# Optimization experiments

Measured on AMD Instinct MI355X. Metric: run time of the kernel, lower is better.

Reference implementation:

```python
import jax, jax.numpy as jnp
import numpy as np

N_BLOCKS = 8
N_WIRES = 24
GAMMA, BETA, ALPHA = 0.1, 0.6, 0.15


def _apply_ry(state, w, theta):
    # RY(theta) = [[cos(t/2), -sin(t/2)], [sin(t/2), cos(t/2)]] on wire w.
    c = jnp.cos(theta * 0.5)
    s = jnp.sin(theta * 0.5)
    st = jnp.moveaxis(state, w, 0)  # (2, ...)
    new = jnp.stack([c * st[0] - s * st[1], s * st[0] + c * st[1]])
    return jnp.moveaxis(new, 0, w)


def _apply_cnot(state, ctrl, tgt):
    # Flip target bit where control bit == 1.
    st = jnp.moveaxis(state, (ctrl, tgt), (0, 1))  # (2, 2, ...)
    new = jnp.stack([st[0], st[1, ::-1]])
    return jnp.moveaxis(new, (0, 1), (ctrl, tgt))


def setup_inputs() -> dict:
    key = jax.random.key(0)
    angles = jax.random.normal(key, (N_BLOCKS, N_WIRES), dtype=jnp.float32)
    return {"angles": angles}


def reference(angles):
    n_blocks, n_wires = angles.shape  # static
    # Initial state |0...0>; RY and CNOT are real, so the state stays real.
    state = jnp.zeros((2,) * n_wires, dtype=angles.dtype).at[(0,) * n_wires].set(1.0)
    for k in range(n_blocks):
        for w in range(n_wires):
            state = _apply_ry(state, w, angles[k, w])
        for w in range(n_wires - 1):  # circular=False -> linear chain
            state = _apply_cnot(state, w, w + 1)
    probs = (state.reshape(-1) ** 2).reshape(2 ** n_wires, 1)  # |amp|^2
    easy_scale = 2.0 ** (n_wires - 1)
    x = (BETA * jnp.tanh(GAMMA * easy_scale * probs)) ** ALPHA
    return x - jnp.mean(x)
```

## Files before the change

kernel.cpp:

```cpp
#include <hip/hip_runtime.h>

#define NB 8
#define SSIZE (1u << 24)


__global__ void k_prep(const float* __restrict__ ang, float* __restrict__ ws) {
    int t = threadIdx.x;
    if (t == 0) ws[0] = 0.0f;
    if (t < NB * 24) {
        float a = 0.5f * ang[t];
        ws[64 + t]  = __builtin_cosf(a);
        ws[256 + t] = __builtin_sinf(a);
    }
}


__device__ __forceinline__ unsigned sw(unsigned f) {
    return f ^ (((f >> 3) ^ (f >> 5)) & 7u);
}

__device__ __forceinline__ void ry2(float& a0, float& a1, float c, float s, bool ctl) {
    float w0 = c * a0 - s * a1;
    float w1 = s * a0 + c * a1;
    a0 = ctl ? w1 : w0;
    a1 = ctl ? w0 : w1;
}

template<int TB, int MODE>
__device__ __forceinline__ void stage8(float4* x, float c, float s) {
#pragma unroll
    for (int j0 = 0; j0 < 8; ++j0) {
        if (j0 & (1 << TB)) continue;
        const int j1 = j0 | (1 << TB);
        const bool ctl = (MODE == 1) || (MODE == 0 && ((j0 >> (TB + 1)) & 1));
        ry2(x[j0].x, x[j1].x, c, s, ctl);
        ry2(x[j0].y, x[j1].y, c, s, ctl);
        ry2(x[j0].z, x[j1].z, c, s, ctl);
        ry2(x[j0].w, x[j1].w, c, s, ctl);
    }
}

__device__ __forceinline__ void coefs(unsigned lane, int lb, bool g,
                                      float c, float s, float& cA, float& cP) {
    bool b = (lane >> lb) & 1u;
    cA = g ? (b ? -s : s) : c;
    cP = g ? c : (b ? s : -s);
}

__device__ __forceinline__ void lane_stage(float4* x, int mask, float cA, float cP) {
#pragma unroll
    for (int j = 0; j < 8; ++j) {
        float px = __shfl_xor(x[j].x, mask, 64);
        float py = __shfl_xor(x[j].y, mask, 64);
        float pz = __shfl_xor(x[j].z, mask, 64);
        float pw = __shfl_xor(x[j].w, mask, 64);
        x[j].x = cA * x[j].x + cP * px;
        x[j].y = cA * x[j].y + cP * py;
        x[j].z = cA * x[j].z + cP * pz;
        x[j].w = cA * x[j].w + cP * pw;
    }
}

__device__ __forceinline__ void lane_stage_jc(float4* x, int mask,
                                              float cA0, float cP0,
                                              float cA1, float cP1) {
#pragma unroll
    for (int j = 0; j < 8; ++j) {
        float cA = (j & 1) ? cA1 : cA0;
        float cP = (j & 1) ? cP1 : cP0;
        float px = __shfl_xor(x[j].x, mask, 64);
        float py = __shfl_xor(x[j].y, mask, 64);
        float pz = __shfl_xor(x[j].z, mask, 64);
        float pw = __shfl_xor(x[j].w, mask, 64);
        x[j].x = cA * x[j].x + cP * px;
        x[j].y = cA * x[j].y + cP * py;
        x[j].z = cA * x[j].z + cP * pz;
        x[j].w = cA * x[j].w + cP * pw;
    }
}

__device__ __forceinline__ void dstages(float4* x, float c1, float s1, bool g1,
                                        float c0, float s0) {
#pragma unroll
    for (int j = 0; j < 8; ++j) {
        ry2(x[j].x, x[j].z, c1, s1, g1);
        ry2(x[j].y, x[j].w, c1, s1, g1);
        ry2(x[j].x, x[j].y, c0, s0, false);
        ry2(x[j].z, x[j].w, c0, s0, true);
    }
}

__device__ __forceinline__ float xform(float v) {
    float z = 838860.8f * v * v;
    float e2 = __builtin_amdgcn_exp2f(z * 2.8853900817779268f);
    float big = 1.0f - 2.0f * __builtin_amdgcn_rcpf(e2 + 1.0f);
    float z2 = z * z;
    float small_ = z * (1.0f - 0.33333333f * z2 * (1.0f - 0.4f * z2));
    float t = (z < 0.04f) ? small_ : big;
    return __builtin_amdgcn_exp2f(0.15f * __builtin_amdgcn_logf(0.6f * t));
}

__global__ __launch_bounds__(512, 4) void k_passA(float* __restrict__ st,
                                                  float* __restrict__ ws,
                                                  int k, int fuse) {
    __shared__ float4 T4[4096];
    const unsigned m = blockIdx.x;
    const unsigned tid = threadIdx.x;
    const unsigned lane = tid & 63u;
    const float* C = ws + 64 + k * 24;
    const float* S = ws + 256 + k * 24;
    float ca[14], sa[14];
#pragma unroll
    for (int b = 0; b < 14; ++b) { ca[b] = C[23 - b]; sa[b] = S[23 - b]; }

    float4* G4 = reinterpret_cast<float4*>(st) + (m << 12);
    float4 x[8];

#pragma unroll
    for (int jj = 0; jj < 8; ++jj) x[jj] = G4[tid + (jj << 9)];
    if (m & 1u) stage8<2, 1>(x, ca[13], sa[13]);
    else        stage8<2,-1>(x, ca[13], sa[13]);
    stage8<1, 0>(x, ca[12], sa[12]);
    stage8<0, 0>(x, ca[11], sa[11]);
#pragma unroll
    for (int jj = 0; jj < 8; ++jj) T4[sw(tid | (jj << 9))] = x[jj];
    __syncthreads();
    const unsigned hi = (tid >> 6) << 9;
#pragma unroll
    for (int jj = 0; jj < 8; ++jj) x[jj] = T4[sw(lane | (jj << 6) | hi)];
    if (tid & 64u) stage8<2, 1>(x, ca[10], sa[10]);
    else           stage8<2,-1>(x, ca[10], sa[10]);
    stage8<1, 0>(x, ca[9], sa[9]);
    stage8<0, 0>(x, ca[8], sa[8]);
    {
        float cA0, cP0, cA1, cP1;
        coefs(lane, 5, false, ca[7], sa[7], cA0, cP0);
        coefs(lane, 5, true,  ca[7], sa[7], cA1, cP1);
        lane_stage_jc(x, 32, cA0, cP0, cA1, cP1);
    }
    { float cA, cP; coefs(lane, 4, (lane >> 5) & 1, ca[6], sa[6], cA, cP); lane_stage(x, 16, cA, cP); }
    { float cA, cP; coefs(lane, 3, (lane >> 4) & 1, ca[5], sa[5], cA, cP); lane_stage(x,  8, cA, cP); }
    { float cA, cP; coefs(lane, 2, (lane >> 3) & 1, ca[4], sa[4], cA, cP); lane_stage(x,  4, cA, cP); }
    { float cA, cP; coefs(lane, 1, (lane >> 2) & 1, ca[3], sa[3], cA, cP); lane_stage(x,  2, cA, cP); }
    { float cA, cP; coefs(lane, 0, (lane >> 1) & 1, ca[2], sa[2], cA, cP); lane_stage(x,  1, cA, cP); }
    dstages(x, ca[1], sa[1], lane & 1u, ca[0], sa[0]);

    if (fuse) {
        float lsum = 0.f;
#pragma unroll
        for (int jj = 0; jj < 8; ++jj) {
            float* v = &x[jj].x;
#pragma unroll
            for (int d = 0; d < 4; ++d) { v[d] = xform(v[d]); lsum += v[d]; }
        }
#pragma unroll
        for (int jj = 0; jj < 8; ++jj) G4[lane | (jj << 6) | hi] = x[jj];
#pragma unroll
        for (int o = 32; o > 0; o >>= 1) lsum += __shfl_down(lsum, o, 64);
        __syncthreads();
        float* wsum = reinterpret_cast<float*>(T4);
        if ((tid & 63u) == 0) wsum[tid >> 6] = lsum;
        __syncthreads();
        if (tid == 0) {
            float b = 0.f;
#pragma unroll
            for (int i = 0; i < 8; ++i) b += wsum[i];
            atomicAdd(ws, b);
        }
    } else {
#pragma unroll
        for (int jj = 0; jj < 8; ++jj) G4[lane | (jj << 6) | hi] = x[jj];
    }
}

__global__ __launch_bounds__(512, 4) void k_passB(float* __restrict__ st,
                                                  const float* __restrict__ ws,
                                                  int k, int init) {
    __shared__ float4 T4[4096];
    const unsigned m = blockIdx.x;
    const unsigned tid = threadIdx.x;
    const unsigned lane = tid & 63u;
    const float* C = ws + 64 + k * 24;
    const float* S = ws + 256 + k * 24;
    float cg[10], sg[10];
#pragma unroll
    for (int t = 0; t < 10; ++t) { cg[t] = C[9 - t]; sg[t] = S[9 - t]; }

    float4* G4 = reinterpret_cast<float4*>(st);
    const unsigned mb = m << 2;
    float4 x[8];

    if (init) {
        const float* C0 = ws + 64;
        const float* S0 = ws + 256;
        float P = 1.f;
        { unsigned g = (tid ^ (tid >> 1)) & 1u;        P *= g ? S0[21] : C0[21]; }
        { unsigned g = ((tid >> 1) ^ m) & 1u;          P *= g ? S0[20] : C0[20]; }
#pragma unroll
        for (int b = 4; b <= 12; ++b) {
            unsigned g = ((m >> (b - 4)) ^ (m >> (b - 3))) & 1u;
            P *= g ? S0[23 - b] : C0[23 - b];
        }
        { unsigned g = ((m >> 9) ^ (tid >> 2)) & 1u;   P *= g ? S0[10] : C0[10]; }
#pragma unroll
        for (int b = 14; b <= 19; ++b) {
            unsigned g = ((tid >> (b - 12)) ^ (tid >> (b - 11))) & 1u;
            P *= g ? S0[23 - b] : C0[23 - b];
        }
        float D[4];
#pragma unroll
        for (int d = 0; d < 4; ++d) {
            unsigned g0 = (d ^ (d >> 1)) & 1u;
            unsigned g1 = ((d >> 1) ^ tid) & 1u;
            D[d] = (g0 ? S0[23] : C0[23]) * (g1 ? S0[22] : C0[22]);
        }
        unsigned t8 = (tid >> 8) & 1u;
#pragma unroll
        for (int jj = 0; jj < 8; ++jj) {
            unsigned g20 = (t8 ^ (unsigned)jj) & 1u;
            unsigned g21 = ((unsigned)jj ^ ((unsigned)jj >> 1)) & 1u;
            unsigned g22 = (((unsigned)jj >> 1) ^ ((unsigned)jj >> 2)) & 1u;
            unsigned g23 = (((unsigned)jj >> 2)) & 1u;
            float J = (g20 ? S0[3] : C0[3]) * (g21 ? S0[2] : C0[2]) *
                      (g22 ? S0[1] : C0[1]) * (g23 ? S0[0] : C0[0]);
            float PJ = P * J;
            x[jj] = make_float4(PJ * D[0], PJ * D[1], PJ * D[2], PJ * D[3]);
        }
    } else {
#pragma unroll
        for (int jj = 0; jj < 8; ++jj) {
            unsigned lf = tid | (jj << 9);
            x[jj] = G4[(lf & 3u) | mb | ((lf >> 2) << 12)];
        }
    }
    stage8<2,-1>(x, cg[9], sg[9]);
    stage8<1, 0>(x, cg[8], sg[8]);
    stage8<0, 0>(x, cg[7], sg[7]);
#pragma unroll
    for (int jj = 0; jj < 8; ++jj) T4[sw(tid | (jj << 9))] = x[jj];
    __syncthreads();
    const unsigned hi = (tid >> 6) << 9;
#pragma unroll
    for (int jj = 0; jj < 8; ++jj) x[jj] = T4[sw(lane | (jj << 6) | hi)];
    if (tid & 64u) stage8<2, 1>(x, cg[6], sg[6]);
    else           stage8<2,-1>(x, cg[6], sg[6]);
    stage8<1, 0>(x, cg[5], sg[5]);
    stage8<0, 0>(x, cg[4], sg[4]);
    {
        float cA0, cP0, cA1, cP1;
        coefs(lane, 5, false, cg[3], sg[3], cA0, cP0);
        coefs(lane, 5, true,  cg[3], sg[3], cA1, cP1);
        lane_stage_jc(x, 32, cA0, cP0, cA1, cP1);
    }
    { float cA, cP; coefs(lane, 4, (lane >> 5) & 1, cg[2], sg[2], cA, cP); lane_stage(x, 16, cA, cP); }
    { float cA, cP; coefs(lane, 3, (lane >> 4) & 1, cg[1], sg[1], cA, cP); lane_stage(x,  8, cA, cP); }
    { float cA, cP; coefs(lane, 2, (lane >> 3) & 1, cg[0], sg[0], cA, cP); lane_stage(x,  4, cA, cP); }
#pragma unroll
    for (int jj = 0; jj < 8; ++jj) {
        unsigned lf = lane | (jj << 6) | hi;
        G4[(lf & 3u) | mb | ((lf >> 2) << 12)] = x[jj];
    }
}

__global__ void k_final(float* __restrict__ st, const float* __restrict__ ws) {
    unsigned idx = blockIdx.x * blockDim.x + threadIdx.x;
    unsigned stride = gridDim.x * blockDim.x;
    float mean = ws[0] * (1.0f / 16777216.0f);
    float4* G4 = reinterpret_cast<float4*>(st);
    for (unsigned q = idx; q < (SSIZE / 4); q += stride) {
        float4 v = G4[q];
        v.x -= mean; v.y -= mean; v.z -= mean; v.w -= mean;
        G4[q] = v;
    }
}

extern "C" void kernel_launch(void* const* d_in, const int* in_sizes, int n_in,
                              void* d_out, int out_size, void* d_ws, size_t ws_size,
                              hipStream_t stream) {
    const float* ang = (const float*)d_in[0];
    float* st = (float*)d_out;
    float* ws = (float*)d_ws;

    k_prep<<<1, 256, 0, stream>>>(ang, ws);
    for (int k = 1; k < NB; ++k) {
        k_passB<<<1024, 512, 0, stream>>>(st, ws, k, (k == 1) ? 1 : 0);
        k_passA<<<1024, 512, 0, stream>>>(st, ws, k, (k == NB - 1) ? 1 : 0);
    }
    k_final<<<4096, 256, 0, stream>>>(st, ws);
}
```

Baseline: 529.8 us.

## Fuse multiple circuit blocks per pass using light-cone ordering, with double-precision state

```diff
diff --git a/kernel.cpp b/kernel.cpp
--- a/kernel.cpp
+++ b/kernel.cpp
@@ -4,13 +4,13 @@
 #define SSIZE (1u << 24)
 
 
-__global__ void k_prep(const float* __restrict__ ang, float* __restrict__ ws) {
+__global__ void k_prep(const float* __restrict__ ang, double* __restrict__ dws) {
     int t = threadIdx.x;
-    if (t == 0) ws[0] = 0.0f;
+    if (t == 0) dws[0] = 0.0;
     if (t < NB * 24) {
-        float a = 0.5f * ang[t];
-        ws[64 + t]  = __builtin_cosf(a);
-        ws[256 + t] = __builtin_sinf(a);
+        double a = 0.5 * (double)ang[t];
+        dws[8 + t]   = cos(a);
+        dws[200 + t] = sin(a);
     }
 }
 
@@ -19,41 +19,41 @@
     return f ^ (((f >> 3) ^ (f >> 5)) & 7u);
 }
 
-__device__ __forceinline__ void ry2(float& a0, float& a1, float c, float s, bool ctl) {
-    float w0 = c * a0 - s * a1;
-    float w1 = s * a0 + c * a1;
+__device__ __forceinline__ void ry2d(double& a0, double& a1, double c, double s, bool ctl) {
+    double w0 = c * a0 - s * a1;
+    double w1 = s * a0 + c * a1;
     a0 = ctl ? w1 : w0;
     a1 = ctl ? w0 : w1;
 }
 
 template<int TB, int MODE>
-__device__ __forceinline__ void stage8(float4* x, float c, float s) {
+__device__ __forceinline__ void stage8d(double4* x, double c, double s) {
 #pragma unroll
     for (int j0 = 0; j0 < 8; ++j0) {
         if (j0 & (1 << TB)) continue;
         const int j1 = j0 | (1 << TB);
         const bool ctl = (MODE == 1) || (MODE == 0 && ((j0 >> (TB + 1)) & 1));
-        ry2(x[j0].x, x[j1].x, c, s, ctl);
-        ry2(x[j0].y, x[j1].y, c, s, ctl);
-        ry2(x[j0].z, x[j1].z, c, s, ctl);
-        ry2(x[j0].w, x[j1].w, c, s, ctl);
-    }
-}
-
-__device__ __forceinline__ void coefs(unsigned lane, int lb, bool g,
-                                      float c, float s, float& cA, float& cP) {
+        ry2d(x[j0].x, x[j1].x, c, s, ctl);
+        ry2d(x[j0].y, x[j1].y, c, s, ctl);
+        ry2d(x[j0].z, x[j1].z, c, s, ctl);
+        ry2d(x[j0].w, x[j1].w, c, s, ctl);
+    }
+}
+
+__device__ __forceinline__ void coefs_d(unsigned lane, int lb, bool g,
+                                        double c, double s, double& cA, double& cP) {
     bool b = (lane >> lb) & 1u;
     cA = g ? (b ? -s : s) : c;
     cP = g ? c : (b ? s : -s);
 }
 
-__device__ __forceinline__ void lane_stage(float4* x, int mask, float cA, float cP) {
+__device__ __forceinline__ void lane_stage_d(double4* x, int mask, double cA, double cP) {
 #pragma unroll
     for (int j = 0; j < 8; ++j) {
-        float px = __shfl_xor(x[j].x, mask, 64);
-        float py = __shfl_xor(x[j].y, mask, 64);
-        float pz = __shfl_xor(x[j].z, mask, 64);
-        float pw = __shfl_xor(x[j].w, mask, 64);
+        double px = __shfl_xor(x[j].x, mask, 64);
+        double py = __shfl_xor(x[j].y, mask, 64);
+        double pz = __shfl_xor(x[j].z, mask, 64);
+        double pw = __shfl_xor(x[j].w, mask, 64);
         x[j].x = cA * x[j].x + cP * px;
         x[j].y = cA * x[j].y + cP * py;
         x[j].z = cA * x[j].z + cP * pz;
@@ -61,17 +61,17 @@
     }
 }
 
-__device__ __forceinline__ void lane_stage_jc(float4* x, int mask,
-                                              float cA0, float cP0,
-                                              float cA1, float cP1) {
+__device__ __forceinline__ void lane_stage_jc_d(double4* x, int mask,
+                                                double cA0, double cP0,
+                                                double cA1, double cP1) {
 #pragma unroll
     for (int j = 0; j < 8; ++j) {
-        float cA = (j & 1) ? cA1 : cA0;
-        float cP = (j & 1) ? cP1 : cP0;
-        float px = __shfl_xor(x[j].x, mask, 64);
-        float py = __shfl_xor(x[j].y, mask, 64);
-        float pz = __shfl_xor(x[j].z, mask, 64);
-        float pw = __shfl_xor(x[j].w, mask, 64);
+        double cA = (j & 1) ? cA1 : cA0;
+        double cP = (j & 1) ? cP1 : cP0;
+        double px = __shfl_xor(x[j].x, mask, 64);
+        double py = __shfl_xor(x[j].y, mask, 64);
+        double pz = __shfl_xor(x[j].z, mask, 64);
+        double pw = __shfl_xor(x[j].w, mask, 64);
         x[j].x = cA * x[j].x + cP * px;
         x[j].y = cA * x[j].y + cP * py;
         x[j].z = cA * x[j].z + cP * pz;
@@ -79,19 +79,18 @@
     }
 }
 
-__device__ __forceinline__ void dstages(float4* x, float c1, float s1, bool g1,
-                                        float c0, float s0) {
+__device__ __forceinline__ void dstages_d(double4* x, double c1, double s1, bool g1,
+                                          double c0, double s0) {
 #pragma unroll
     for (int j = 0; j < 8; ++j) {
-        ry2(x[j].x, x[j].z, c1, s1, g1);
-        ry2(x[j].y, x[j].w, c1, s1, g1);
-        ry2(x[j].x, x[j].y, c0, s0, false);
-        ry2(x[j].z, x[j].w, c0, s0, true);
-    }
-}
-
-__device__ __forceinline__ float xform(float v) {
-    float z = 838860.8f * v * v;
+        ry2d(x[j].x, x[j].z, c1, s1, g1);
+        ry2d(x[j].y, x[j].w, c1, s1, g1);
+        ry2d(x[j].x, x[j].y, c0, s0, false);
+        ry2d(x[j].z, x[j].w, c0, s0, true);
+    }
+}
+
+__device__ __forceinline__ float xform(float z) {
     float e2 = __builtin_amdgcn_exp2f(z * 2.8853900817779268f);
     float big = 1.0f - 2.0f * __builtin_amdgcn_rcpf(e2 + 1.0f);
     float z2 = z * z;
@@ -100,118 +99,126 @@
     return __builtin_amdgcn_exp2f(0.15f * __builtin_amdgcn_logf(0.6f * t));
 }
 
-__global__ __launch_bounds__(512, 4) void k_passA(float* __restrict__ st,
-                                                  float* __restrict__ ws,
-                                                  int k, int fuse) {
+
+__device__ __forceinline__ float4 lo4(const double4 v) {
+    return make_float4(__int_as_float(__double2loint(v.x)),
+                       __int_as_float(__double2loint(v.y)),
+                       __int_as_float(__double2loint(v.z)),
+                       __int_as_float(__double2loint(v.w)));
+}
+__device__ __forceinline__ float4 hi4(const double4 v) {
+    return make_float4(__int_as_float(__double2hiint(v.x)),
+                       __int_as_float(__double2hiint(v.y)),
+                       __int_as_float(__double2hiint(v.z)),
+                       __int_as_float(__double2hiint(v.w)));
+}
+__device__ __forceinline__ double4 mk4(const float4 h, const float4 l) {
+    return make_double4(__hiloint2double(__float_as_int(h.x), __float_as_int(l.x)),
+                        __hiloint2double(__float_as_int(h.y), __float_as_int(l.y)),
+                        __hiloint2double(__float_as_int(h.z), __float_as_int(l.z)),
+                        __hiloint2double(__float_as_int(h.w), __float_as_int(l.w)));
+}
+
+__device__ __forceinline__ void t_fwd_d(float4* T4, double4* x, unsigned tid,
+                                        unsigned lane, unsigned hi, bool protect) {
+    if (protect) __syncthreads();
+#pragma unroll
+    for (int jj = 0; jj < 8; ++jj) T4[sw(tid | (jj << 9))] = lo4(x[jj]);
+    __syncthreads();
+    float4 tl[8];
+#pragma unroll
+    for (int jj = 0; jj < 8; ++jj) tl[jj] = T4[sw(lane | (jj << 6) | hi)];
+    __syncthreads();
+#pragma unroll
+    for (int jj = 0; jj < 8; ++jj) T4[sw(tid | (jj << 9))] = hi4(x[jj]);
+    __syncthreads();
+#pragma unroll
+    for (int jj = 0; jj < 8; ++jj)
+        x[jj] = mk4(T4[sw(lane | (jj << 6) | hi)], tl[jj]);
+}
+
+__device__ __forceinline__ void t_back_d(float4* T4, double4* x, unsigned tid,
+                                         unsigned lane, unsigned hi) {
+    __syncthreads();
+#pragma unroll
+    for (int jj = 0; jj < 8; ++jj) T4[sw(lane | (jj << 6) | hi)] = lo4(x[jj]);
+    __syncthreads();
+    float4 tl[8];
+#pragma unroll
+    for (int jj = 0; jj < 8; ++jj) tl[jj] = T4[sw(tid | (jj << 9))];
+    __syncthreads();
+#pragma unroll
+    for (int jj = 0; jj < 8; ++jj) T4[sw(lane | (jj << 6) | hi)] = hi4(x[jj]);
+    __syncthreads();
+#pragma unroll
+    for (int jj = 0; jj < 8; ++jj)
+        x[jj] = mk4(T4[sw(tid | (jj << 9))], tl[jj]);
+}
+
+__device__ __forceinline__ void jj_trio_d(double4* x, const double* c, const double* s,
+                                          bool top_on, int start) {
+    if (start == 0) {
+        if (top_on) stage8d<2, 1>(x, c[0], s[0]);
+        else        stage8d<2,-1>(x, c[0], s[0]);
+    }
+    if (start <= 1) stage8d<1, 0>(x, c[1], s[1]);
+    stage8d<0, 0>(x, c[2], s[2]);
+}
+
+__device__ __forceinline__ void lane_ladder_d(double4* x, unsigned lane,
+                                              const double* c, const double* s, int n) {
+    {
+        double cA0, cP0, cA1, cP1;
+        coefs_d(lane, 5, false, c[0], s[0], cA0, cP0);
+        coefs_d(lane, 5, true,  c[0], s[0], cA1, cP1);
+        lane_stage_jc_d(x, 32, cA0, cP0, cA1, cP1);
+    }
+    if (n > 1) { double cA, cP; coefs_d(lane, 4, (lane >> 5) & 1, c[1], s[1], cA, cP); lane_stage_d(x, 16, cA, cP); }
+    if (n > 2) { double cA, cP; coefs_d(lane, 3, (lane >> 4) & 1, c[2], s[2], cA, cP); lane_stage_d(x,  8, cA, cP); }
+    if (n > 3) { double cA, cP; coefs_d(lane, 2, (lane >> 3) & 1, c[3], s[3], cA, cP); lane_stage_d(x,  4, cA, cP); }
+    if (n > 4) { double cA, cP; coefs_d(lane, 1, (lane >> 2) & 1, c[4], s[4], cA, cP); lane_stage_d(x,  2, cA, cP); }
+    if (n > 5) { double cA, cP; coefs_d(lane, 0, (lane >> 1) & 1, c[5], s[5], cA, cP); lane_stage_d(x,  1, cA, cP); }
+}
+
+__device__ __forceinline__ double4 d4_of(const float4 f) {
+    return make_double4((double)f.x, (double)f.y, (double)f.z, (double)f.w);
+}
+__device__ __forceinline__ float4 f4_of(const double4 d) {
+    return make_float4((float)d.x, (float)d.y, (float)d.z, (float)d.w);
+}
+
+__global__ __launch_bounds__(512, 2) void k_H(float* __restrict__ st,
+                                              const double* __restrict__ dws,
+                                              int kbase, int nblk, int init) {
     __shared__ float4 T4[4096];
-    const unsigned m = blockIdx.x;
+    const unsigned bid = blockIdx.x;
+    const unsigned m = (bid >> 3) | ((bid & 7u) << 7);
     const unsigned tid = threadIdx.x;
     const unsigned lane = tid & 63u;
-    const float* C = ws + 64 + k * 24;
-    const float* S = ws + 256 + k * 24;
-    float ca[14], sa[14];
-#pragma unroll
-    for (int b = 0; b < 14; ++b) { ca[b] = C[23 - b]; sa[b] = S[23 - b]; }
-
-    float4* G4 = reinterpret_cast<float4*>(st) + (m << 12);
-    float4 x[8];
-
-#pragma unroll
-    for (int jj = 0; jj < 8; ++jj) x[jj] = G4[tid + (jj << 9)];
-    if (m & 1u) stage8<2, 1>(x, ca[13], sa[13]);
-    else        stage8<2,-1>(x, ca[13], sa[13]);
-    stage8<1, 0>(x, ca[12], sa[12]);
-    stage8<0, 0>(x, ca[11], sa[11]);
-#pragma unroll
-    for (int jj = 0; jj < 8; ++jj) T4[sw(tid | (jj << 9))] = x[jj];
-    __syncthreads();
     const unsigned hi = (tid >> 6) << 9;
-#pragma unroll
-    for (int jj = 0; jj < 8; ++jj) x[jj] = T4[sw(lane | (jj << 6) | hi)];
-    if (tid & 64u) stage8<2, 1>(x, ca[10], sa[10]);
-    else           stage8<2,-1>(x, ca[10], sa[10]);
-    stage8<1, 0>(x, ca[9], sa[9]);
-    stage8<0, 0>(x, ca[8], sa[8]);
-    {
-        float cA0, cP0, cA1, cP1;
-        coefs(lane, 5, false, ca[7], sa[7], cA0, cP0);
-        coefs(lane, 5, true,  ca[7], sa[7], cA1, cP1);
-        lane_stage_jc(x, 32, cA0, cP0, cA1, cP1);
-    }
-    { float cA, cP; coefs(lane, 4, (lane >> 5) & 1, ca[6], sa[6], cA, cP); lane_stage(x, 16, cA, cP); }
-    { float cA, cP; coefs(lane, 3, (lane >> 4) & 1, ca[5], sa[5], cA, cP); lane_stage(x,  8, cA, cP); }
-    { float cA, cP; coefs(lane, 2, (lane >> 3) & 1, ca[4], sa[4], cA, cP); lane_stage(x,  4, cA, cP); }
-    { float cA, cP; coefs(lane, 1, (lane >> 2) & 1, ca[3], sa[3], cA, cP); lane_stage(x,  2, cA, cP); }
-    { float cA, cP; coefs(lane, 0, (lane >> 1) & 1, ca[2], sa[2], cA, cP); lane_stage(x,  1, cA, cP); }
-    dstages(x, ca[1], sa[1], lane & 1u, ca[0], sa[0]);
-
-    if (fuse) {
-        float lsum = 0.f;
-#pragma unroll
-        for (int jj = 0; jj < 8; ++jj) {
-            float* v = &x[jj].x;
-#pragma unroll
-            for (int d = 0; d < 4; ++d) { v[d] = xform(v[d]); lsum += v[d]; }
-        }
-#pragma unroll
-        for (int jj = 0; jj < 8; ++jj) G4[lane | (jj << 6) | hi] = x[jj];
-#pragma unroll
-        for (int o = 32; o > 0; o >>= 1) lsum += __shfl_down(lsum, o, 64);
-        __syncthreads();
-        float* wsum = reinterpret_cast<float*>(T4);
-        if ((tid & 63u) == 0) wsum[tid >> 6] = lsum;
-        __syncthreads();
-        if (tid == 0) {
-            float b = 0.f;
-#pragma unroll
-            for (int i = 0; i < 8; ++i) b += wsum[i];
-            atomicAdd(ws, b);
-        }
-    } else {
-#pragma unroll
-        for (int jj = 0; jj < 8; ++jj) G4[lane | (jj << 6) | hi] = x[jj];
-    }
-}
-
-__global__ __launch_bounds__(512, 4) void k_passB(float* __restrict__ st,
-                                                  const float* __restrict__ ws,
-                                                  int k, int init) {
-    __shared__ float4 T4[4096];
-    const unsigned m = blockIdx.x;
-    const unsigned tid = threadIdx.x;
-    const unsigned lane = tid & 63u;
-    const float* C = ws + 64 + k * 24;
-    const float* S = ws + 256 + k * 24;
-    float cg[10], sg[10];
-#pragma unroll
-    for (int t = 0; t < 10; ++t) { cg[t] = C[9 - t]; sg[t] = S[9 - t]; }
-
     float4* G4 = reinterpret_cast<float4*>(st);
-    const unsigned mb = m << 2;
-    float4 x[8];
+    double4 x[8];
 
     if (init) {
-        const float* C0 = ws + 64;
-        const float* S0 = ws + 256;
-        float P = 1.f;
-        { unsigned g = (tid ^ (tid >> 1)) & 1u;        P *= g ? S0[21] : C0[21]; }
-        { unsigned g = ((tid >> 1) ^ m) & 1u;          P *= g ? S0[20] : C0[20]; }
-#pragma unroll
-        for (int b = 4; b <= 12; ++b) {
-            unsigned g = ((m >> (b - 4)) ^ (m >> (b - 3))) & 1u;
+        const double* C0 = dws + 8;
+        const double* S0 = dws + 200;
+        double P = 1.0;
+#pragma unroll
+        for (int b = 2; b <= 10; ++b) {
+            unsigned g = ((m >> (b - 2)) ^ (m >> (b - 1))) & 1u;
             P *= g ? S0[23 - b] : C0[23 - b];
         }
-        { unsigned g = ((m >> 9) ^ (tid >> 2)) & 1u;   P *= g ? S0[10] : C0[10]; }
-#pragma unroll
-        for (int b = 14; b <= 19; ++b) {
+        { unsigned g = ((m >> 9) ^ tid) & 1u; P *= g ? S0[12] : C0[12]; }
+#pragma unroll
+        for (int b = 12; b <= 19; ++b) {
             unsigned g = ((tid >> (b - 12)) ^ (tid >> (b - 11))) & 1u;
             P *= g ? S0[23 - b] : C0[23 - b];
         }
-        float D[4];
+        double D[4];
 #pragma unroll
         for (int d = 0; d < 4; ++d) {
             unsigned g0 = (d ^ (d >> 1)) & 1u;
-            unsigned g1 = ((d >> 1) ^ tid) & 1u;
+            unsigned g1 = ((d >> 1) ^ m) & 1u;
             D[d] = (g0 ? S0[23] : C0[23]) * (g1 ? S0[22] : C0[22]);
         }
         unsigned t8 = (tid >> 8) & 1u;
@@ -221,51 +228,97 @@
             unsigned g21 = ((unsigned)jj ^ ((unsigned)jj >> 1)) & 1u;
             unsigned g22 = (((unsigned)jj >> 1) ^ ((unsigned)jj >> 2)) & 1u;
             unsigned g23 = (((unsigned)jj >> 2)) & 1u;
-            float J = (g20 ? S0[3] : C0[3]) * (g21 ? S0[2] : C0[2]) *
-                      (g22 ? S0[1] : C0[1]) * (g23 ? S0[0] : C0[0]);
-            float PJ = P * J;
-            x[jj] = make_float4(PJ * D[0], PJ * D[1], PJ * D[2], PJ * D[3]);
+            double J = (g20 ? S0[3] : C0[3]) * (g21 ? S0[2] : C0[2]) *
+                       (g22 ? S0[1] : C0[1]) * (g23 ? S0[0] : C0[0]);
+            double PJ = P * J;
+            x[jj] = make_double4(PJ * D[0], PJ * D[1], PJ * D[2], PJ * D[3]);
         }
     } else {
 #pragma unroll
         for (int jj = 0; jj < 8; ++jj) {
-            unsigned lf = tid | (jj << 9);
-            x[jj] = G4[(lf & 3u) | mb | ((lf >> 2) << 12)];
-        }
-    }
-    stage8<2,-1>(x, cg[9], sg[9]);
-    stage8<1, 0>(x, cg[8], sg[8]);
-    stage8<0, 0>(x, cg[7], sg[7]);
-#pragma unroll
-    for (int jj = 0; jj < 8; ++jj) T4[sw(tid | (jj << 9))] = x[jj];
-    __syncthreads();
+            unsigned w = tid | (jj << 9);
+            x[jj] = d4_of(G4[m | (w << 10)]);
+        }
+    }
+
+    for (int i = 0; i < nblk; ++i) {
+        const double* C = dws + 8   + (kbase + i) * 24;
+        const double* S = dws + 200 + (kbase + i) * 24;
+        jj_trio_d(x, C + 0, S + 0, false, 0);
+        t_fwd_d(T4, x, tid, lane, hi, i > 0);
+        jj_trio_d(x, C + 3, S + 3, (tid & 64u) != 0, 0);
+        lane_ladder_d(x, lane, C + 6, S + 6, 6 - i);
+        if (i < nblk - 1) t_back_d(T4, x, tid, lane, hi);
+    }
+#pragma unroll
+    for (int jj = 0; jj < 8; ++jj) {
+        unsigned w = lane | (jj << 6) | hi;
+        G4[m | (w << 10)] = f4_of(x[jj]);
+    }
+}
+
+__global__ __launch_bounds__(512, 2) void k_L(float* __restrict__ st,
+                                              double* __restrict__ dws,
+                                              int kbase, int nblk, int fuse) {
+    __shared__ float4 T4[4096];
+    const unsigned m = blockIdx.x;
+    const unsigned tid = threadIdx.x;
+    const unsigned lane = tid & 63u;
     const unsigned hi = (tid >> 6) << 9;
-#pragma unroll
-    for (int jj = 0; jj < 8; ++jj) x[jj] = T4[sw(lane | (jj << 6) | hi)];
-    if (tid & 64u) stage8<2, 1>(x, cg[6], sg[6]);
-    else           stage8<2,-1>(x, cg[6], sg[6]);
-    stage8<1, 0>(x, cg[5], sg[5]);
-    stage8<0, 0>(x, cg[4], sg[4]);
-    {
-        float cA0, cP0, cA1, cP1;
-        coefs(lane, 5, false, cg[3], sg[3], cA0, cP0);
-        coefs(lane, 5, true,  cg[3], sg[3], cA1, cP1);
-        lane_stage_jc(x, 32, cA0, cP0, cA1, cP1);
-    }
-    { float cA, cP; coefs(lane, 4, (lane >> 5) & 1, cg[2], sg[2], cA, cP); lane_stage(x, 16, cA, cP); }
-    { float cA, cP; coefs(lane, 3, (lane >> 4) & 1, cg[1], sg[1], cA, cP); lane_stage(x,  8, cA, cP); }
-    { float cA, cP; coefs(lane, 2, (lane >> 3) & 1, cg[0], sg[0], cA, cP); lane_stage(x,  4, cA, cP); }
-#pragma unroll
-    for (int jj = 0; jj < 8; ++jj) {
-        unsigned lf = lane | (jj << 6) | hi;
-        G4[(lf & 3u) | mb | ((lf >> 2) << 12)] = x[jj];
-    }
-}
-
-__global__ void k_final(float* __restrict__ st, const float* __restrict__ ws) {
+    float4* G4 = reinterpret_cast<float4*>(st) + (m << 12);
+    double4 x[8];
+#pragma unroll
+    for (int jj = 0; jj < 8; ++jj) x[jj] = d4_of(G4[tid + (jj << 9)]);
+
+    for (int i = 0; i < nblk; ++i) {
+        const double* C = dws + 8   + (kbase + i) * 24;
+        const double* S = dws + 200 + (kbase + i) * 24;
+        jj_trio_d(x, C + 10, S + 10, (m & 1u) != 0, 2 - i);
+        t_fwd_d(T4, x, tid, lane, hi, i > 0);
+        jj_trio_d(x, C + 13, S + 13, (tid & 64u) != 0, 0);
+        lane_ladder_d(x, lane, C + 16, S + 16, 6);
+        dstages_d(x, C[22], S[22], lane & 1u, C[23], S[23]);
+        if (i < nblk - 1) t_back_d(T4, x, tid, lane, hi);
+    }
+
+    if (fuse) {
+        double lsum = 0.0;
+#pragma unroll
+        for (int jj = 0; jj < 8; ++jj) {
+            double* v = &x[jj].x;
+            float4 o;
+            float* ov = &o.x;
+#pragma unroll
+            for (int d = 0; d < 4; ++d) {
+                float z = (float)(838860.8 * v[d] * v[d]);
+                float xf = xform(z);
+                ov[d] = xf;
+                lsum += (double)xf;
+            }
+            G4[lane | (jj << 6) | hi] = o;
+        }
+#pragma unroll
+        for (int o = 32; o > 0; o >>= 1) lsum += __shfl_down(lsum, o, 64);
+        __syncthreads();
+        double* wsum = reinterpret_cast<double*>(T4);
+        if ((tid & 63u) == 0) wsum[tid >> 6] = lsum;
+        __syncthreads();
+        if (tid == 0) {
+            double b = 0.0;
+#pragma unroll
+            for (int i = 0; i < 8; ++i) b += wsum[i];
+            atomicAdd(dws, b);
+        }
+    } else {
+#pragma unroll
+        for (int jj = 0; jj < 8; ++jj) G4[lane | (jj << 6) | hi] = f4_of(x[jj]);
+    }
+}
+
+__global__ void k_final(float* __restrict__ st, const double* __restrict__ dws) {
     unsigned idx = blockIdx.x * blockDim.x + threadIdx.x;
     unsigned stride = gridDim.x * blockDim.x;
-    float mean = ws[0] * (1.0f / 16777216.0f);
+    float mean = (float)(dws[0] * (1.0 / 16777216.0));
     float4* G4 = reinterpret_cast<float4*>(st);
     for (unsigned q = idx; q < (SSIZE / 4); q += stride) {
         float4 v = G4[q];
@@ -279,12 +332,14 @@
                               hipStream_t stream) {
     const float* ang = (const float*)d_in[0];
     float* st = (float*)d_out;
-    float* ws = (float*)d_ws;
-
-    k_prep<<<1, 256, 0, stream>>>(ang, ws);
-    for (int k = 1; k < NB; ++k) {
-        k_passB<<<1024, 512, 0, stream>>>(st, ws, k, (k == 1) ? 1 : 0);
-        k_passA<<<1024, 512, 0, stream>>>(st, ws, k, (k == NB - 1) ? 1 : 0);
-    }
-    k_final<<<4096, 256, 0, stream>>>(st, ws);
-}
+    double* dws = (double*)d_ws;
+
+    k_prep<<<1, 256, 0, stream>>>(ang, dws);
+    k_H<<<1024, 512, 0, stream>>>(st, dws, 1, 3, 1);
+    k_L<<<1024, 512, 0, stream>>>(st, dws, 1, 3, 0);
+    k_H<<<1024, 512, 0, stream>>>(st, dws, 4, 3, 0);
+    k_L<<<1024, 512, 0, stream>>>(st, dws, 4, 3, 0);
+    k_H<<<1024, 512, 0, stream>>>(st, dws, 7, 1, 0);
+    k_L<<<1024, 512, 0, stream>>>(st, dws, 7, 1, 1);
+    k_final<<<4096, 256, 0, stream>>>(st, dws);
+}
```

Result: slower. 759.8 us (+43.4%).
